# Kernel optimization log

Measured on AMD Instinct MI355X. Metric: run time of the kernel, lower is better.

## Reference

```python
import jax, jax.numpy as jnp
import numpy as np

B, S, D_MODEL, D_K, D_V = 8, 2048, 1024, 64, 64
NEG = -1e9


def setup_inputs() -> dict:
    key = jax.random.key(0)
    ks = jax.random.split(key, 12)
    inv = 1.0 / np.sqrt(D_MODEL)
    return {
        "q": jax.random.normal(ks[0], (B, S, D_MODEL), jnp.float32),
        "k": jax.random.normal(ks[1], (B, S, D_MODEL), jnp.float32),
        "v": jax.random.normal(ks[2], (B, S, D_MODEL), jnp.float32),
        "mask": jax.random.randint(ks[3], (1, S, S), 0, 2, jnp.int32),
        # Linear weights stored as [in, out] so y = x @ W + b
        "Wq": jax.random.normal(ks[4], (D_MODEL, D_K), jnp.float32) * inv,
        "bq": jnp.zeros((D_K,), jnp.float32),
        "Wk": jax.random.normal(ks[5], (D_MODEL, D_K), jnp.float32) * inv,
        "bk": jnp.zeros((D_K,), jnp.float32),
        "Wv": jax.random.normal(ks[6], (D_MODEL, D_V), jnp.float32) * inv,
        "bv": jnp.zeros((D_V,), jnp.float32),
        "Wo": jax.random.normal(ks[7], (D_V, D_MODEL), jnp.float32) * (1.0 / np.sqrt(D_V)),
        "bo": jnp.zeros((D_MODEL,), jnp.float32),
    }


def reference(q, k, v, mask, Wq, bq, Wk, bk, Wv, bv, Wo, bo):
    # single-head projections: [b, s, d_model] -> [b, s, d_k/d_v]
    qp = q @ Wq + bq
    kp = k @ Wk + bk
    vp = v @ Wv + bv
    # UNSCALED dot-product scores (original has no 1/sqrt(d_k)): [b, s, s]
    scores = jnp.einsum("bqd,bkd->bqk", qp, kp)
    scores = jnp.where(mask == 0, jnp.float32(NEG), scores)
    attn = jax.nn.softmax(scores, axis=-1)  # dropout p=0.0 -> identity
    out = jnp.einsum("bqk,bkv->bqv", attn, vp)
    return out @ Wo + bo
```

## Files before the change

### kernel.cpp

```cpp
#include <hip/hip_runtime.h>
#include <hip/hip_bf16.h>

typedef __bf16 bf16_t;
typedef __attribute__((ext_vector_type(8))) __bf16 bf16x8;
typedef __attribute__((ext_vector_type(4))) float f32x4;

#define MFMA16(a, b, c) __builtin_amdgcn_mfma_f32_16x16x32_bf16((a), (b), (c), 0, 0, 0)

#define NB 8
#define SS 2048
#define DM 1024
#define DK 64
#define NROW (NB * SS)
#define NSPLIT 4
#define SPLEN (SS / NSPLIT)

typedef __attribute__((address_space(1))) const unsigned int ga_u32;
typedef __attribute__((address_space(3))) unsigned int ls_u32;
#define GLOAD16(g, l) \
  __builtin_amdgcn_global_load_lds((ga_u32*)(g), (ls_u32*)(l), 16, 0, 0)

union U16x8 { unsigned short u[8]; uint4 q; };
union U16x4 { unsigned short u[4]; ushort4 v; };

__device__ inline void split_hl(float x, unsigned short& h, unsigned short& l) {
  bf16_t hb = (bf16_t)x;
  bf16_t lb = (bf16_t)(x - (float)hb);
  h = *(unsigned short*)&hb;
  l = *(unsigned short*)&lb;
}

__global__ __launch_bounds__(256) void maskpack_kernel(
    const int* __restrict__ mask, unsigned int* __restrict__ mbits) {
  int idx = blockIdx.x * 256 + threadIdx.x;
  int q = idx >> 6, w = idx & 63;
  const int4* src = (const int4*)(mask + (q << 11) + (w << 5));
  unsigned int bits = 0u;
#pragma unroll
  for (int i = 0; i < 8; ++i) {
    int4 t = src[i];
    bits |= (t.x != 0 ? 1u : 0u) << (i * 4 + 0);
    bits |= (t.y != 0 ? 1u : 0u) << (i * 4 + 1);
    bits |= (t.z != 0 ? 1u : 0u) << (i * 4 + 2);
    bits |= (t.w != 0 ? 1u : 0u) << (i * 4 + 3);
  }
  mbits[idx] = bits;
}

__global__ __launch_bounds__(256) void wprep_kernel(
    const float* __restrict__ Wq, const float* __restrict__ Wk,
    const float* __restrict__ Wv, char* __restrict__ wimg) {
  int which = blockIdx.x >> 6;
  const float* W = which == 0 ? Wq : (which == 1 ? Wk : Wv);
  char* img = wimg + (size_t)which * 16 * 16384;
  int e = (blockIdx.x & 63) * 256 + threadIdx.x;
  int k = e >> 4, n0 = (e & 15) << 2;
  float4 f = *(const float4*)(W + k * 64 + n0);
  float fv[4] = {f.x, f.y, f.z, f.w};
  char* base = img + (k >> 6) * 16384;
  int kk = k & 63;
#pragma unroll
  for (int u = 0; u < 4; ++u) {
    int n = n0 + u;
    unsigned short h, l;
    split_hl(fv[u], h, l);
    int byte = n * 128 + ((2 * kk) ^ ((n & 7) << 4));
    *(unsigned short*)(base + byte) = h;
    *(unsigned short*)(base + 8192 + byte) = l;
  }
}

__global__ __launch_bounds__(256) void proj3_kernel(
    const float* __restrict__ qx, const float* __restrict__ kx,
    const float* __restrict__ vx, const char* __restrict__ wimg,
    const float* __restrict__ bq, const float* __restrict__ bk,
    const float* __restrict__ bv, bf16_t* __restrict__ qhi,
    bf16_t* __restrict__ qlo, char* __restrict__ kimg,
    char* __restrict__ vimg) {
  __shared__ __align__(16) char smem[49152];
  char* xbuf = smem;
  const int mode = blockIdx.y;
  const float* X = mode == 0 ? qx : (mode == 1 ? kx : vx);
  const float* bias = mode == 0 ? bq : (mode == 1 ? bk : bv);
  const int tid = threadIdx.x;
  const int lane = tid & 63;
  const int wv = tid >> 6;
  const int lr = lane & 15;
  const int g = lane >> 4;
  const int rbase = blockIdx.x * 64;
  const int xr = tid >> 2;
  const int kg = (tid & 3) << 4;
  const int row_local = wv * 16 + lr;
  const int swa = (row_local & 7) << 4;
  const int swx = (xr & 7) << 4;

  f32x4 acc[4] = {};
  const char* wsrc0 = wimg + (size_t)mode * 16 * 16384;

  float4 xa, xb, xc, xd;
  auto issueX = [&](int ch) {
    const float4* xp =
        (const float4*)(X + (size_t)(rbase + xr) * DM + ch * 64 + kg);
    xa = xp[0]; xb = xp[1]; xc = xp[2]; xd = xp[3];
  };
  auto writeX = [&]() {
    float xv[16] = {xa.x, xa.y, xa.z, xa.w, xb.x, xb.y, xb.z, xb.w,
                    xc.x, xc.y, xc.z, xc.w, xd.x, xd.y, xd.z, xd.w};
    U16x8 hq[2], lq[2];
#pragma unroll
    for (int i = 0; i < 16; ++i)
      split_hl(xv[i], hq[i >> 3].u[i & 7], lq[i >> 3].u[i & 7]);
    char* xh = xbuf + xr * 128;
    int b0 = 2 * kg;
    *(uint4*)(xh + (b0 ^ swx)) = hq[0].q;
    *(uint4*)(xh + ((b0 + 16) ^ swx)) = hq[1].q;
    *(uint4*)(xh + 8192 + (b0 ^ swx)) = lq[0].q;
    *(uint4*)(xh + 8192 + ((b0 + 16) ^ swx)) = lq[1].q;
  };
  auto stageW = [&](int ch, char* dst) {
    const char* wsrc = wsrc0 + ch * 16384;
#pragma unroll
    for (int u = 0; u < 4; ++u)
      GLOAD16(wsrc + u * 4096 + tid * 16, dst + u * 4096 + tid * 16);
  };
  auto compute = [&](const char* wb) {
#pragma unroll
    for (int ks = 0; ks < 2; ++ks) {
      int co = ks * 64 + g * 16;
      bf16x8 ah = *(const bf16x8*)(xbuf + row_local * 128 + (co ^ swa));
      bf16x8 al = *(const bf16x8*)(xbuf + 8192 + row_local * 128 + (co ^ swa));
#pragma unroll
      for (int c = 0; c < 4; ++c) {
        int n = c * 16 + lr;
        int swb = (n & 7) << 4;
        bf16x8 bh = *(const bf16x8*)(wb + n * 128 + (co ^ swb));
        bf16x8 bl = *(const bf16x8*)(wb + 8192 + n * 128 + (co ^ swb));
        acc[c] = MFMA16(ah, bl, acc[c]);
        acc[c] = MFMA16(al, bh, acc[c]);
        acc[c] = MFMA16(ah, bh, acc[c]);
      }
    }
  };

  issueX(0);
  stageW(0, smem + 16384);
  writeX();
  issueX(1);
  asm volatile("s_waitcnt vmcnt(4)" ::: "memory");
  asm volatile("s_waitcnt lgkmcnt(0)" ::: "memory");
  __builtin_amdgcn_s_barrier();
  __builtin_amdgcn_sched_barrier(0);

  for (int ch = 0; ch < 16; ++ch) {
    char* wc = (ch & 1) ? smem + 32768 : smem + 16384;
    char* wn = (ch & 1) ? smem + 16384 : smem + 32768;
    if (ch < 15) stageW(ch + 1, wn);
    compute(wc);
    if (ch < 15) {
      __builtin_amdgcn_sched_barrier(0);
      __builtin_amdgcn_s_barrier();
      __builtin_amdgcn_sched_barrier(0);
      writeX();
      if (ch < 14) {
        issueX(ch + 2);
        asm volatile("s_waitcnt vmcnt(4)" ::: "memory");
      } else {
        asm volatile("s_waitcnt vmcnt(0)" ::: "memory");
      }
      asm volatile("s_waitcnt lgkmcnt(0)" ::: "memory");
      __builtin_amdgcn_s_barrier();
      __builtin_amdgcn_sched_barrier(0);
    }
  }
  __syncthreads();
  float* sacc = (float*)smem;
#pragma unroll
  for (int c = 0; c < 4; ++c)
#pragma unroll
    for (int j = 0; j < 4; ++j)
      sacc[(wv * 16 + g * 4 + j) * 69 + c * 16 + lr] = acc[c][j];
  __syncthreads();

  const int b = rbase >> 11;
  const int t = (rbase & (SS - 1)) >> 6;
  if (mode == 0) {
    int r = tid & 63, cg = tid >> 6;
    int row = rbase + r;
    U16x8 h0, h1, l0, l1;
#pragma unroll
    for (int i = 0; i < 16; ++i) {
      float v = sacc[r * 69 + cg * 16 + i] + bias[cg * 16 + i];
      if (i < 8) split_hl(v, h0.u[i & 7], l0.u[i & 7]);
      else       split_hl(v, h1.u[i & 7], l1.u[i & 7]);
    }
    *(uint4*)((char*)qhi + (size_t)row * 128 + cg * 32) = h0.q;
    *(uint4*)((char*)qhi + (size_t)row * 128 + cg * 32 + 16) = h1.q;
    *(uint4*)((char*)qlo + (size_t)row * 128 + cg * 32) = l0.q;
    *(uint4*)((char*)qlo + (size_t)row * 128 + cg * 32 + 16) = l1.q;
  } else if (mode == 1) {
    int r = tid & 63, cg = tid >> 6;
    char* base = kimg + (((size_t)(b * 32 + t)) << 14);
    int sw = (r & 7) << 4;
#pragma unroll
    for (int m = 0; m < 4; ++m) {
      U16x4 hv, lv;
#pragma unroll
      for (int u = 0; u < 4; ++u) {
        int col = cg * 16 + m * 4 + u;
        float v = sacc[r * 69 + col] + bias[col];
        split_hl(v, hv.u[u], lv.u[u]);
      }
      int off = (cg * 32 + m * 8) ^ sw;
      *(ushort4*)(base + r * 128 + off) = hv.v;
      *(ushort4*)(base + 8192 + r * 128 + off) = lv.v;
    }
  } else {
    int d = tid & 63, rg = tid >> 6;
    char* base = vimg + (((size_t)(b * 32 + t)) << 14);
    int sw = (d & 7) << 4;
    float bv = bias[d];
#pragma unroll
    for (int m = 0; m < 4; ++m) {
      U16x4 hv, lv;
#pragma unroll
      for (int u = 0; u < 4; ++u) {
        int r = rg * 16 + m * 4 + u;
        float v = sacc[r * 69 + d] + bv;
        split_hl(v, hv.u[u], lv.u[u]);
      }
      int off = (rg * 32 + m * 8) ^ sw;
      *(ushort4*)(base + d * 128 + off) = hv.v;
      *(ushort4*)(base + 8192 + d * 128 + off) = lv.v;
    }
  }
}

__global__ __launch_bounds__(256) void attn_kernel(
    const bf16_t* __restrict__ qhi, const bf16_t* __restrict__ qlo,
    const char* __restrict__ kimg, const char* __restrict__ vimg,
    const unsigned int* __restrict__ mbits, float* __restrict__ part_acc,
    float* __restrict__ part_m, float* __restrict__ part_l) {
  __shared__ __align__(16) char kbuf[16384];
  __shared__ __align__(16) char vbuf[16384];
  __shared__ __align__(16) char plds_all[4][2048];
  const int tid = threadIdx.x;
  const int lane = tid & 63;
  const int wv = tid >> 6;
  const int lr = lane & 15;
  const int g = lane >> 4;
  char* plds = &plds_all[wv][0];
  const int qrow0 = (blockIdx.x * 4 + wv) * 16;
  const int split = blockIdx.y;
  const int kv0 = split * SPLEN;
  const int b = qrow0 >> 11;
  const int sq0 = (qrow0 & (SS - 1)) + g * 4;

  const bf16_t* qh = qhi + (qrow0 + lr) * DK + g * 8;
  const bf16_t* ql = qlo + (qrow0 + lr) * DK + g * 8;
  bf16x8 qh0 = *(const bf16x8*)qh;
  bf16x8 qh1 = *(const bf16x8*)(qh + 32);
  bf16x8 ql0 = *(const bf16x8*)ql;
  bf16x8 ql1 = *(const bf16x8*)(ql + 32);

  float m[4], lsum[4];
  f32x4 acc[4] = {};
#pragma unroll
  for (int j = 0; j < 4; ++j) { m[j] = -3.0e38f; lsum[j] = 0.f; }

  for (int it = 0; it < SPLEN / 64; ++it) {
    const int tglob = (kv0 >> 6) + it;
    const char* ksrc = kimg + (((size_t)(b * 32 + tglob)) << 14);
    const char* vsrc = vimg + (((size_t)(b * 32 + tglob)) << 14);
#pragma unroll
    for (int u = 0; u < 4; ++u) {
      GLOAD16(ksrc + tid * 16 + u * 4096, kbuf + tid * 16 + u * 4096);
      GLOAD16(vsrc + tid * 16 + u * 4096, vbuf + tid * 16 + u * 4096);
    }
    asm volatile("s_waitcnt vmcnt(0)\n" ::: "memory");
    __syncthreads();
    f32x4 sac[4];
#pragma unroll
    for (int t = 0; t < 4; ++t) {
      int rk = t * 16 + lr;
      int sw = (rk & 7) << 4;
      bf16x8 kh0 = *(const bf16x8*)(kbuf + rk * 128 + ((g * 16) ^ sw));
      bf16x8 kh1 = *(const bf16x8*)(kbuf + rk * 128 + ((64 + g * 16) ^ sw));
      bf16x8 kl0 = *(const bf16x8*)(kbuf + 8192 + rk * 128 + ((g * 16) ^ sw));
      bf16x8 kl1 =
          *(const bf16x8*)(kbuf + 8192 + rk * 128 + ((64 + g * 16) ^ sw));
      f32x4 s = {};
      s = MFMA16(qh0, kl0, s);
      s = MFMA16(qh1, kl1, s);
      s = MFMA16(ql0, kh0, s);
      s = MFMA16(ql1, kh1, s);
      s = MFMA16(qh0, kh0, s);
      s = MFMA16(qh1, kh1, s);
      sac[t] = s;
    }
    const int wbase = (kv0 >> 5) + it * 2;
    uint2 m2[4];
#pragma unroll
    for (int j = 0; j < 4; ++j)
      m2[j] = *(const uint2*)(mbits + (sq0 + j) * 64 + wbase);
#pragma unroll
    for (int t = 0; t < 4; ++t)
#pragma unroll
      for (int j = 0; j < 4; ++j) {
        unsigned w = (t & 2) ? m2[j].y : m2[j].x;
        if (!((w >> ((t & 1) * 16 + lr)) & 1u)) sac[t][j] = -1e9f;
      }
#pragma unroll
    for (int j = 0; j < 4; ++j) {
      float v = sac[0][j];
#pragma unroll
      for (int t = 1; t < 4; ++t) v = fmaxf(v, sac[t][j]);
      v = fmaxf(v, __shfl_xor(v, 1, 64));
      v = fmaxf(v, __shfl_xor(v, 2, 64));
      v = fmaxf(v, __shfl_xor(v, 4, 64));
      v = fmaxf(v, __shfl_xor(v, 8, 64));
      float mn = fmaxf(m[j], v);
      float sc = __expf(m[j] - mn);
      m[j] = mn;
      lsum[j] *= sc;
#pragma unroll
      for (int c = 0; c < 4; ++c) acc[c][j] *= sc;
    }
    float ps[4] = {0.f, 0.f, 0.f, 0.f};
#pragma unroll
    for (int t = 0; t < 4; ++t)
#pragma unroll
      for (int j = 0; j < 4; ++j) {
        float p = __expf(sac[t][j] - m[j]);
        bf16_t pb = (bf16_t)p;
        ps[j] += (float)pb;
        int row = g * 4 + j;
        int byte = row * 128 + (((t * 16 + lr) * 2) ^ ((row & 7) << 4));
        *(bf16_t*)(plds + byte) = pb;
      }
#pragma unroll
    for (int j = 0; j < 4; ++j) {
      float s_ = ps[j];
      s_ += __shfl_xor(s_, 1, 64);
      s_ += __shfl_xor(s_, 2, 64);
      s_ += __shfl_xor(s_, 4, 64);
      s_ += __shfl_xor(s_, 8, 64);
      lsum[j] += s_;
    }
    asm volatile("s_waitcnt lgkmcnt(0)\n" ::: "memory");
#pragma unroll
    for (int kt = 0; kt < 2; ++kt) {
      int pbyte = lr * 128 + ((kt * 64 + g * 16) ^ ((lr & 7) << 4));
      bf16x8 pa = *(const bf16x8*)(plds + pbyte);
#pragma unroll
      for (int c = 0; c < 4; ++c) {
        int n = c * 16 + lr;
        int swv = (n & 7) << 4;
        bf16x8 vfh = *(const bf16x8*)(vbuf + n * 128 + ((kt * 64 + g * 16) ^ swv));
        bf16x8 vfl =
            *(const bf16x8*)(vbuf + 8192 + n * 128 + ((kt * 64 + g * 16) ^ swv));
        acc[c] = MFMA16(pa, vfh, acc[c]);
        acc[c] = MFMA16(pa, vfl, acc[c]);
      }
    }
    __syncthreads();
  }
#pragma unroll
  for (int c = 0; c < 4; ++c)
#pragma unroll
    for (int j = 0; j < 4; ++j)
      part_acc[((size_t)split * NROW + qrow0 + g * 4 + j) * DK + c * 16 + lr] =
          acc[c][j];
  if (lr == 0) {
#pragma unroll
    for (int j = 0; j < 4; ++j) {
      part_m[split * NROW + qrow0 + g * 4 + j] = m[j];
      part_l[split * NROW + qrow0 + g * 4 + j] = lsum[j];
    }
  }
}

__global__ __launch_bounds__(256) void combine_kernel(
    const float* __restrict__ pacc, const float* __restrict__ pm,
    const float* __restrict__ pl, float* __restrict__ attn_f) {
  int idx = blockIdx.x * 256 + threadIdx.x;
  int row = idx >> 6;
  float m0 = pm[row], m1 = pm[NROW + row];
  float m2 = pm[2 * NROW + row], m3 = pm[3 * NROW + row];
  float M = fmaxf(fmaxf(m0, m1), fmaxf(m2, m3));
  float w0 = __expf(m0 - M), w1 = __expf(m1 - M);
  float w2 = __expf(m2 - M), w3 = __expf(m3 - M);
  float l = w0 * pl[row] + w1 * pl[NROW + row] + w2 * pl[2 * NROW + row] +
            w3 * pl[3 * NROW + row];
  float a = w0 * pacc[idx] + w1 * pacc[(size_t)NROW * DK + idx] +
            w2 * pacc[2 * (size_t)NROW * DK + idx] +
            w3 * pacc[3 * (size_t)NROW * DK + idx];
  attn_f[idx] = a / l;
}

__global__ __launch_bounds__(256) void oproj_kernel(
    const float* __restrict__ attn, const float* __restrict__ Wo,
    const float* __restrict__ bo, float* __restrict__ out) {
  __shared__ __align__(16) bf16_t wt[256 * 64];
  const int tid = threadIdx.x;
  const int lane = tid & 63;
  const int wv = tid >> 6;
  const int lr = lane & 15;
  const int g = lane >> 4;
  const int rbase = blockIdx.x * 64 + wv * 16;
  const int c0 = blockIdx.y * 256;
  {
    const int k = tid >> 2;
    const int n0 = (tid & 3) << 6;
    const float4* src = (const float4*)(Wo + k * DM + c0 + n0);
#pragma unroll
    for (int i = 0; i < 16; ++i) {
      float4 f = src[i];
      float fv[4] = {f.x, f.y, f.z, f.w};
#pragma unroll
      for (int u = 0; u < 4; ++u) {
        int n = n0 + i * 4 + u;
        int byte = (n << 7) + (k << 1);
        byte ^= (n & 7) << 4;
        *(bf16_t*)((char*)wt + byte) = (bf16_t)fv[u];
      }
    }
  }
  __syncthreads();
  const float* ab = attn + (rbase + lr) * DK + g * 8;
  float4 x0 = *(const float4*)ab;
  float4 x1 = *(const float4*)(ab + 4);
  float4 y0 = *(const float4*)(ab + 32);
  float4 y1 = *(const float4*)(ab + 36);
  float xv[8] = {x0.x, x0.y, x0.z, x0.w, x1.x, x1.y, x1.z, x1.w};
  float yv[8] = {y0.x, y0.y, y0.z, y0.w, y1.x, y1.y, y1.z, y1.w};
  bf16x8 ah0, al0, ah1, al1;
#pragma unroll
  for (int i = 0; i < 8; ++i) {
    ah0[i] = (bf16_t)xv[i];
    al0[i] = (bf16_t)(xv[i] - (float)ah0[i]);
    ah1[i] = (bf16_t)yv[i];
    al1[i] = (bf16_t)(yv[i] - (float)ah1[i]);
  }
  f32x4 acc[16] = {};
#pragma unroll
  for (int c = 0; c < 16; ++c) {
    int n = c * 16 + lr;
    int byte0 = (n << 7) + ((g * 8) << 1);
    byte0 ^= (n & 7) << 4;
    int byte1 = (n << 7) + ((32 + g * 8) << 1);
    byte1 ^= (n & 7) << 4;
    bf16x8 b0 = *(const bf16x8*)((const char*)wt + byte0);
    bf16x8 b1 = *(const bf16x8*)((const char*)wt + byte1);
    acc[c] = MFMA16(ah0, b0, acc[c]);
    acc[c] = MFMA16(al0, b0, acc[c]);
    acc[c] = MFMA16(ah1, b1, acc[c]);
    acc[c] = MFMA16(al1, b1, acc[c]);
  }
#pragma unroll
  for (int c = 0; c < 16; ++c) {
    float bv = bo[c0 + c * 16 + lr];
#pragma unroll
    for (int j = 0; j < 4; ++j)
      out[(rbase + g * 4 + j) * DM + c0 + c * 16 + lr] = acc[c][j] + bv;
  }
}

extern "C" void kernel_launch(void* const* d_in, const int* in_sizes, int n_in,
                              void* d_out, int out_size, void* d_ws,
                              size_t ws_size, hipStream_t stream) {
  const float* q = (const float*)d_in[0];
  const float* k = (const float*)d_in[1];
  const float* v = (const float*)d_in[2];
  const int* mask = (const int*)d_in[3];
  const float* Wq = (const float*)d_in[4];
  const float* bq = (const float*)d_in[5];
  const float* Wk = (const float*)d_in[6];
  const float* bk = (const float*)d_in[7];
  const float* Wv = (const float*)d_in[8];
  const float* bv = (const float*)d_in[9];
  const float* Wo = (const float*)d_in[10];
  const float* bo = (const float*)d_in[11];
  float* out = (float*)d_out;

  bf16_t* qhi = (bf16_t*)d_ws;
  bf16_t* qlo = qhi + (size_t)NROW * DK;
  char* kimg = (char*)(qlo + (size_t)NROW * DK);
  char* vimg = kimg + ((size_t)NB * 32 << 14);
  char* wimg = vimg + ((size_t)NB * 32 << 14);
  float* part_acc = (float*)(wimg + (size_t)3 * 16 * 16384);
  float* part_m = part_acc + (size_t)NSPLIT * NROW * DK;
  float* part_l = part_m + (size_t)NSPLIT * NROW;
  float* attn_f = part_l + (size_t)NSPLIT * NROW;
  unsigned int* mbits = (unsigned int*)(attn_f + (size_t)NROW * DK);

  maskpack_kernel<<<dim3(SS * (SS / 32) / 256), dim3(256), 0, stream>>>(mask,
                                                                        mbits);
  wprep_kernel<<<dim3(192), dim3(256), 0, stream>>>(Wq, Wk, Wv, wimg);
  proj3_kernel<<<dim3(NROW / 64, 3), dim3(256), 0, stream>>>(
      q, k, v, wimg, bq, bk, bv, qhi, qlo, kimg, vimg);
  attn_kernel<<<dim3(NROW / 64, NSPLIT), dim3(256), 0, stream>>>(
      qhi, qlo, kimg, vimg, mbits, part_acc, part_m, part_l);
  combine_kernel<<<dim3(NROW * DK / 256), dim3(256), 0, stream>>>(
      part_acc, part_m, part_l, attn_f);
  oproj_kernel<<<dim3(NROW / 64, DM / 256), dim3(256), 0, stream>>>(attn_f, Wo,
                                                                    bo, out);
}
```

Baseline: 140.6 us.

## Load X directly into MFMA A-operand registers, dropping LDS staging

The projection kernel now loads each lane's slice of the activation rows straight from global memory into registers in the MFMA A-operand layout, double-buffered across chunks. The hi/lo bf16 split happens in registers rather than after a round trip through LDS. This removes the X LDS buffer, its writes and reads, and one barrier per chunk, and shrinks shared memory from 48KB to 32KB, which may raise occupancy. In exchange it adds register pressure from two in-flight X slots and full unrolling, and the global loads are less coalesced (16-byte pieces strided by row).

```diff
diff --git a/kernel.cpp b/kernel.cpp
--- a/kernel.cpp
+++ b/kernel.cpp
@@ -77,8 +77,7 @@
     const float* __restrict__ bv, bf16_t* __restrict__ qhi,
     bf16_t* __restrict__ qlo, char* __restrict__ kimg,
     char* __restrict__ vimg) {
-  __shared__ __align__(16) char smem[49152];
-  char* xbuf = smem;
+  __shared__ __align__(16) char smem[32768];
   const int mode = blockIdx.y;
   const float* X = mode == 0 ? qx : (mode == 1 ? kx : vx);
   const float* bias = mode == 0 ? bq : (mode == 1 ? bk : bv);
@@ -88,34 +87,19 @@
   const int lr = lane & 15;
   const int g = lane >> 4;
   const int rbase = blockIdx.x * 64;
-  const int xr = tid >> 2;
-  const int kg = (tid & 3) << 4;
-  const int row_local = wv * 16 + lr;
-  const int swa = (row_local & 7) << 4;
-  const int swx = (xr & 7) << 4;
 
   f32x4 acc[4] = {};
   const char* wsrc0 = wimg + (size_t)mode * 16 * 16384;
-
-  float4 xa, xb, xc, xd;
-  auto issueX = [&](int ch) {
-    const float4* xp =
-        (const float4*)(X + (size_t)(rbase + xr) * DM + ch * 64 + kg);
-    xa = xp[0]; xb = xp[1]; xc = xp[2]; xd = xp[3];
-  };
-  auto writeX = [&]() {
-    float xv[16] = {xa.x, xa.y, xa.z, xa.w, xb.x, xb.y, xb.z, xb.w,
-                    xc.x, xc.y, xc.z, xc.w, xd.x, xd.y, xd.z, xd.w};
-    U16x8 hq[2], lq[2];
-#pragma unroll
-    for (int i = 0; i < 16; ++i)
-      split_hl(xv[i], hq[i >> 3].u[i & 7], lq[i >> 3].u[i & 7]);
-    char* xh = xbuf + xr * 128;
-    int b0 = 2 * kg;
-    *(uint4*)(xh + (b0 ^ swx)) = hq[0].q;
-    *(uint4*)(xh + ((b0 + 16) ^ swx)) = hq[1].q;
-    *(uint4*)(xh + 8192 + (b0 ^ swx)) = lq[0].q;
-    *(uint4*)(xh + 8192 + ((b0 + 16) ^ swx)) = lq[1].q;
+  const float* xsrc = X + (size_t)(rbase + wv * 16 + lr) * DM + g * 8;
+
+  float4 xr[2][4];
+
+  auto issueX = [&](int ch, int slot) {
+    const float4* xp = (const float4*)(xsrc + ch * 64);
+    xr[slot][0] = xp[0];
+    xr[slot][1] = xp[1];
+    xr[slot][2] = xp[8];
+    xr[slot][3] = xp[9];
   };
   auto stageW = [&](int ch, char* dst) {
     const char* wsrc = wsrc0 + ch * 16384;
@@ -123,51 +107,58 @@
     for (int u = 0; u < 4; ++u)
       GLOAD16(wsrc + u * 4096 + tid * 16, dst + u * 4096 + tid * 16);
   };
-  auto compute = [&](const char* wb) {
+
+  issueX(0, 0);
+  stageW(0, smem);
+  issueX(1, 1);
+  asm volatile("s_waitcnt vmcnt(4)" ::: "memory");
+  __builtin_amdgcn_s_barrier();
+  __builtin_amdgcn_sched_barrier(0);
+
+#pragma unroll
+  for (int ch = 0; ch < 16; ++ch) {
+    char* wc = (ch & 1) ? smem + 16384 : smem;
+    char* wn = (ch & 1) ? smem : smem + 16384;
+    if (ch < 15) stageW(ch + 1, wn);
+    bf16x8 ah[2], al[2];
+#pragma unroll
+    for (int ks = 0; ks < 2; ++ks) {
+      float xv[8];
+#pragma unroll
+      for (int u = 0; u < 4; ++u) {
+        xv[u] = ((const float*)&xr[ch & 1][ks * 2])[u];
+        xv[4 + u] = ((const float*)&xr[ch & 1][ks * 2 + 1])[u];
+      }
+#pragma unroll
+      for (int i = 0; i < 8; ++i) {
+        unsigned short h, l;
+        split_hl(xv[i], h, l);
+        ((unsigned short*)&ah[ks])[i] = h;
+        ((unsigned short*)&al[ks])[i] = l;
+      }
+    }
+    if (ch < 14) issueX(ch + 2, ch & 1);
 #pragma unroll
     for (int ks = 0; ks < 2; ++ks) {
       int co = ks * 64 + g * 16;
-      bf16x8 ah = *(const bf16x8*)(xbuf + row_local * 128 + (co ^ swa));
-      bf16x8 al = *(const bf16x8*)(xbuf + 8192 + row_local * 128 + (co ^ swa));
 #pragma unroll
       for (int c = 0; c < 4; ++c) {
         int n = c * 16 + lr;
         int swb = (n & 7) << 4;
-        bf16x8 bh = *(const bf16x8*)(wb + n * 128 + (co ^ swb));
-        bf16x8 bl = *(const bf16x8*)(wb + 8192 + n * 128 + (co ^ swb));
-        acc[c] = MFMA16(ah, bl, acc[c]);
-        acc[c] = MFMA16(al, bh, acc[c]);
-        acc[c] = MFMA16(ah, bh, acc[c]);
-      }
-    }
-  };
-
-  issueX(0);
-  stageW(0, smem + 16384);
-  writeX();
-  issueX(1);
-  asm volatile("s_waitcnt vmcnt(4)" ::: "memory");
-  asm volatile("s_waitcnt lgkmcnt(0)" ::: "memory");
-  __builtin_amdgcn_s_barrier();
-  __builtin_amdgcn_sched_barrier(0);
-
-  for (int ch = 0; ch < 16; ++ch) {
-    char* wc = (ch & 1) ? smem + 32768 : smem + 16384;
-    char* wn = (ch & 1) ? smem + 16384 : smem + 32768;
-    if (ch < 15) stageW(ch + 1, wn);
-    compute(wc);
+        bf16x8 bh = *(const bf16x8*)(wc + n * 128 + (co ^ swb));
+        bf16x8 bl = *(const bf16x8*)(wc + 8192 + n * 128 + (co ^ swb));
+        acc[c] = MFMA16(ah[ks], bl, acc[c]);
+        acc[c] = MFMA16(al[ks], bh, acc[c]);
+        acc[c] = MFMA16(ah[ks], bh, acc[c]);
+      }
+    }
     if (ch < 15) {
       __builtin_amdgcn_sched_barrier(0);
-      __builtin_amdgcn_s_barrier();
-      __builtin_amdgcn_sched_barrier(0);
-      writeX();
       if (ch < 14) {
-        issueX(ch + 2);
         asm volatile("s_waitcnt vmcnt(4)" ::: "memory");
       } else {
         asm volatile("s_waitcnt vmcnt(0)" ::: "memory");
       }
-      asm volatile("s_waitcnt lgkmcnt(0)" ::: "memory");
       __builtin_amdgcn_s_barrier();
       __builtin_amdgcn_sched_barrier(0);
     }
```

New measurement: 146.5 us. 4.2% more time.

## Overlap next K/V tile loads with compute and remap block order

Applied to the files above, without the earlier changes.

Splits the K and V tile loads into separate staging steps. The next K tile is issued once the current QK^T MFMAs finish, and the next V tile once the PV MFMAs finish, so global-to-LDS copies run underneath softmax and matmul work instead of stalling at the top of each iteration. Partial vmcnt waits plus extra barriers protect buffer reuse. Block indices are also permuted so that consecutive blocks touch different batches, which changes how L2 and cache locality is spread. The cost is more barriers per iteration and the reliance on exact vmcnt counting, since each stage issues 4 loads per thread.

```diff
diff --git a/kernel.cpp b/kernel.cpp
--- a/kernel.cpp
+++ b/kernel.cpp
@@ -249,11 +249,14 @@
   const int lr = lane & 15;
   const int g = lane >> 4;
   char* plds = &plds_all[wv][0];
-  const int qrow0 = (blockIdx.x * 4 + wv) * 16;
+  const int bx = blockIdx.x;
+  const int sx = (bx & 7) * 32 + (bx >> 3);
+  const int qrow0 = (sx * 4 + wv) * 16;
   const int split = blockIdx.y;
   const int kv0 = split * SPLEN;
   const int b = qrow0 >> 11;
   const int sq0 = (qrow0 & (SS - 1)) + g * 4;
+  const int t0 = kv0 >> 6;
 
   const bf16_t* qh = qhi + (qrow0 + lr) * DK + g * 8;
   const bf16_t* ql = qlo + (qrow0 + lr) * DK + g * 8;
@@ -262,22 +265,32 @@
   bf16x8 ql0 = *(const bf16x8*)ql;
   bf16x8 ql1 = *(const bf16x8*)(ql + 32);
 
+  auto stageK = [&](int t2) {
+    const char* ksrc = kimg + (((size_t)(b * 32 + t0 + t2)) << 14);
+#pragma unroll
+    for (int u = 0; u < 4; ++u)
+      GLOAD16(ksrc + tid * 16 + u * 4096, kbuf + tid * 16 + u * 4096);
+  };
+  auto stageV = [&](int t2) {
+    const char* vsrc = vimg + (((size_t)(b * 32 + t0 + t2)) << 14);
+#pragma unroll
+    for (int u = 0; u < 4; ++u)
+      GLOAD16(vsrc + tid * 16 + u * 4096, vbuf + tid * 16 + u * 4096);
+  };
+
   float m[4], lsum[4];
   f32x4 acc[4] = {};
 #pragma unroll
   for (int j = 0; j < 4; ++j) { m[j] = -3.0e38f; lsum[j] = 0.f; }
 
+  stageK(0);
+  stageV(0);
+  __builtin_amdgcn_sched_barrier(0);
+
   for (int it = 0; it < SPLEN / 64; ++it) {
-    const int tglob = (kv0 >> 6) + it;
-    const char* ksrc = kimg + (((size_t)(b * 32 + tglob)) << 14);
-    const char* vsrc = vimg + (((size_t)(b * 32 + tglob)) << 14);
-#pragma unroll
-    for (int u = 0; u < 4; ++u) {
-      GLOAD16(ksrc + tid * 16 + u * 4096, kbuf + tid * 16 + u * 4096);
-      GLOAD16(vsrc + tid * 16 + u * 4096, vbuf + tid * 16 + u * 4096);
-    }
-    asm volatile("s_waitcnt vmcnt(0)\n" ::: "memory");
-    __syncthreads();
+    asm volatile("s_waitcnt vmcnt(4)" ::: "memory");
+    __builtin_amdgcn_s_barrier();
+    __builtin_amdgcn_sched_barrier(0);
     f32x4 sac[4];
 #pragma unroll
     for (int t = 0; t < 4; ++t) {
@@ -297,11 +310,16 @@
       s = MFMA16(qh1, kh1, s);
       sac[t] = s;
     }
+    __builtin_amdgcn_sched_barrier(0);
+    __builtin_amdgcn_s_barrier();
+    __builtin_amdgcn_sched_barrier(0);
     const int wbase = (kv0 >> 5) + it * 2;
     uint2 m2[4];
 #pragma unroll
     for (int j = 0; j < 4; ++j)
       m2[j] = *(const uint2*)(mbits + (sq0 + j) * 64 + wbase);
+    if (it < SPLEN / 64 - 1) stageK(it + 1);
+    __builtin_amdgcn_sched_barrier(0);
 #pragma unroll
     for (int t = 0; t < 4; ++t)
 #pragma unroll
@@ -347,6 +365,12 @@
       lsum[j] += s_;
     }
     asm volatile("s_waitcnt lgkmcnt(0)\n" ::: "memory");
+    if (it < SPLEN / 64 - 1)
+      asm volatile("s_waitcnt vmcnt(4)" ::: "memory");
+    else
+      asm volatile("s_waitcnt vmcnt(0)" ::: "memory");
+    __builtin_amdgcn_s_barrier();
+    __builtin_amdgcn_sched_barrier(0);
 #pragma unroll
     for (int kt = 0; kt < 2; ++kt) {
       int pbyte = lr * 128 + ((kt * 64 + g * 16) ^ ((lr & 7) << 4));
@@ -362,7 +386,11 @@
         acc[c] = MFMA16(pa, vfl, acc[c]);
       }
     }
-    __syncthreads();
+    __builtin_amdgcn_sched_barrier(0);
+    __builtin_amdgcn_s_barrier();
+    __builtin_amdgcn_sched_barrier(0);
+    if (it < SPLEN / 64 - 1) stageV(it + 1);
+    __builtin_amdgcn_sched_barrier(0);
   }
 #pragma unroll
   for (int c = 0; c < 4; ++c)
```

New measurement: 142.6 us. About the same (+1.4%).
